# Performance work log

Hardware: AMD Instinct MI355X
Metric: run time of the kernel (lower is better)

The kernel has to match this reference:

```python
import jax, jax.numpy as jnp
import numpy as np

N, D_IN, D_OUT, RANK, MAX_LORAS = 4096, 2048, 2048, 16, 32


def setup_inputs() -> dict:
    key = jax.random.key(0)
    ks = jax.random.split(key, 6)
    x = jax.random.normal(ks[0], (N, D_IN), dtype=jnp.float32)
    adapter_ids = jax.random.randint(ks[1], (N,), 0, MAX_LORAS, dtype=jnp.int32)
    W_base = jax.random.normal(ks[2], (D_OUT, D_IN), dtype=jnp.float32) * (D_IN ** -0.5)
    b_base = jax.random.normal(ks[3], (D_OUT,), dtype=jnp.float32) * 0.01
    lora_A = jax.random.normal(ks[4], (MAX_LORAS, RANK, D_IN), dtype=jnp.float32) * (D_IN ** -0.5)
    lora_B = jax.random.normal(ks[5], (MAX_LORAS, D_OUT, RANK), dtype=jnp.float32) * (RANK ** -0.5)
    lora_scaling = jnp.ones((MAX_LORAS,), dtype=jnp.float32)
    return {"x": x, "adapter_ids": adapter_ids, "W_base": W_base, "b_base": b_base,
            "lora_A": lora_A, "lora_B": lora_B, "lora_scaling": lora_scaling}


def reference(x, adapter_ids, W_base, b_base, lora_A, lora_B, lora_scaling):
    previous_dtype = x.dtype
    # base_layer(x): dense Linear
    result = x @ W_base.T + b_base                      # [N, D_OUT]
    # lora_A(x, adapter_ids): per-token gathered low-rank down-projection (bgmv)
    A_w = lora_A[adapter_ids]                           # [N, RANK, D_IN]
    A_result = jnp.einsum('ni,nri->nr', x, A_w)         # [N, RANK]
    # lora_B(A_result, adapter_ids): per-token gathered up-projection
    B_w = lora_B[adapter_ids]                           # [N, D_OUT, RANK]
    B_result = jnp.einsum('nr,nor->no', A_result, B_w)  # [N, D_OUT]
    # scaled residual add, per-adapter scaling
    scaling = lora_scaling[adapter_ids][:, None]        # [N, 1]
    result = result + B_result * scaling
    # cast back to input dtype (skip_dtype_convert=False)
    return result.astype(previous_dtype)
```

## Files before the change

kernel.cpp:

```cpp
#include <hip/hip_runtime.h>
#include <hip/hip_bf16.h>
#include <stdint.h>

#define NTOK 4096
#define DIN  2048
#define DOUT 2048
#define RANK 16
#define NLORA 32
#define LCAP 512

typedef __attribute__((ext_vector_type(4))) float f32x4;
typedef __attribute__((ext_vector_type(8))) _Float16 f16x8;

typedef const __attribute__((address_space(1))) void* gas_ptr;
typedef __attribute__((address_space(3))) void* las_ptr;

__global__ __launch_bounds__(256)
void prep_kernel(const float* __restrict__ x, const int* __restrict__ ids,
                 const float* __restrict__ W, const float* __restrict__ lA,
                 const float* __restrict__ lB,
                 _Float16* __restrict__ xh, _Float16* __restrict__ wh,
                 _Float16* __restrict__ lAh, _Float16* __restrict__ lBh,
                 int* __restrict__ list, int* __restrict__ counts) {
    const int bid = blockIdx.x;
    if (bid < 7168) {
        const float* src; _Float16* dst; int lb;
        if      (bid < 2048) { src = W;  dst = wh;  lb = bid; }
        else if (bid < 6144) { src = x;  dst = xh;  lb = bid - 2048; }
        else if (bid < 6656) { src = lA; dst = lAh; lb = bid - 6144; }
        else                 { src = lB; dst = lBh; lb = bid - 6656; }
        const size_t i = ((size_t)lb * 256 + threadIdx.x) * 8;
        f32x4 a = *(const f32x4*)(src + i);
        f32x4 b = *(const f32x4*)(src + i + 4);
        f16x8 h;
        h[0] = (_Float16)a.x; h[1] = (_Float16)a.y; h[2] = (_Float16)a.z; h[3] = (_Float16)a.w;
        h[4] = (_Float16)b.x; h[5] = (_Float16)b.y; h[6] = (_Float16)b.z; h[7] = (_Float16)b.w;
        *(f16x8*)(dst + i) = h;
        return;
    }
    const int a = bid - 7168;
    const int wv = threadIdx.x >> 6;
    const int lane = threadIdx.x & 63;
    __shared__ int wcnt[4];
    int c = 0;
    for (int t0 = wv * 1024; t0 < wv * 1024 + 1024; t0 += 64)
        c += __popcll(__ballot(ids[t0 + lane] == a));
    if (lane == 0) wcnt[wv] = c;
    __syncthreads();
    int off = 0;
    for (int w = 0; w < wv; w++) off += wcnt[w];
    if (threadIdx.x == 0) counts[a] = wcnt[0] + wcnt[1] + wcnt[2] + wcnt[3];
    for (int t0 = wv * 1024; t0 < wv * 1024 + 1024; t0 += 64) {
        const int t = t0 + lane;
        const bool m = (ids[t] == a);
        unsigned long long bal = __ballot(m);
        if (m) {
            int pos = off + __popcll(bal & ((1ULL << lane) - 1));
            if (pos < LCAP) list[a * LCAP + pos] = t;
        }
        off += __popcll(bal);
    }
}

__global__ __launch_bounds__(512)
void lora_fused_kernel(const _Float16* __restrict__ xh, const _Float16* __restrict__ lAh,
                       const _Float16* __restrict__ lBh, const float* __restrict__ bias,
                       const float* __restrict__ scal, const int* __restrict__ list,
                       const int* __restrict__ counts, _Float16* __restrict__ Bresh) {
    const int a = blockIdx.x, tile = blockIdx.y;
    const int cnt = counts[a];
    if (tile * 16 >= cnt) return;
    const int wave = threadIdx.x >> 6;
    const int lane = threadIdx.x & 63;
    const int fr = lane & 15, fq = lane >> 4;

    __shared__ float red[8][256];
    __shared__ _Float16 ares_h[16 * 16];

    const int idxA = tile * 16 + fr;
    const int tA = (idxA < cnt) ? list[a * LCAP + idxA] : list[a * LCAP];

    const _Float16* xr = xh + (size_t)tA * DIN + wave * 256 + fq * 8;
    const _Float16* ar = lAh + (size_t)a * RANK * DIN + fr * DIN + wave * 256 + fq * 8;
    f32x4 acc = (f32x4){0.f, 0.f, 0.f, 0.f};
#pragma unroll
    for (int st = 0; st < 8; st++) {
        f16x8 af = *(const f16x8*)(xr + st * 32);
        f16x8 bf = *(const f16x8*)(ar + st * 32);
        acc = __builtin_amdgcn_mfma_f32_16x16x32_f16(af, bf, acc, 0, 0, 0);
    }
#pragma unroll
    for (int j = 0; j < 4; j++) red[wave][lane * 4 + j] = acc[j];
    __syncthreads();
    if (wave == 0) {
        const float s = scal[a];
#pragma unroll
        for (int j = 0; j < 4; j++) {
            float v = 0.f;
#pragma unroll
            for (int w = 0; w < 8; w++) v += red[w][lane * 4 + j];
            ares_h[(fq * 4 + j) * RANK + fr] = (_Float16)(v * s);
        }
    }
    __syncthreads();

    f16x8 af = {};
    if (fq < 2) af = *(const f16x8*)(ares_h + fr * RANK + fq * 8);
    int tj[4];
#pragma unroll
    for (int j = 0; j < 4; j++) {
        const int idx = tile * 16 + fq * 4 + j;
        tj[j] = (idx < cnt) ? list[a * LCAP + idx] : -1;
    }
    const _Float16* Bb = lBh + (size_t)a * DOUT * RANK;
#pragma unroll 4
    for (int oi = 0; oi < 16; oi++) {
        const int o = (wave * 16 + oi) * 16 + fr;
        f16x8 bf = {};
        if (fq < 2) bf = *(const f16x8*)(Bb + (size_t)o * RANK + fq * 8);
        f32x4 c = (f32x4){0.f, 0.f, 0.f, 0.f};
        c = __builtin_amdgcn_mfma_f32_16x16x32_f16(af, bf, c, 0, 0, 0);
        const float bv = bias[o];
#pragma unroll
        for (int j = 0; j < 4; j++)
            if (tj[j] >= 0) Bresh[(size_t)tj[j] * DOUT + o] = (_Float16)(c[j] + bv);
    }
}

#define GBK 64
#define NT (DIN / GBK)

__global__ __launch_bounds__(256, 2)
void gemm_kernel(const _Float16* __restrict__ Ah, const _Float16* __restrict__ Wh,
                 const _Float16* __restrict__ Bresh, float* __restrict__ out) {
    extern __shared__ _Float16 sm[];
    _Float16* As = sm;
    _Float16* Bs = sm + 16384;

    const int tid = threadIdx.x;
    const int wave = tid >> 6;
    const int lane = tid & 63;
    const int wr = wave >> 1, wc = wave & 1;

    const int p = blockIdx.x;
    const int L = (p & 7) * 64 + (p >> 3);
    const int bm = (L >> 4) * 128;
    const int bn = (L & 15) * 128;

    const int rsub = lane >> 3;
    const int cch = (lane & 7) ^ rsub;
    const _Float16* srcA[4];
    const _Float16* srcB[4];
#pragma unroll
    for (int i = 0; i < 4; i++) {
        const int row = (wave * 4 + i) * 8 + rsub;
        srcA[i] = Ah + (size_t)(bm + row) * DIN + cch * 8;
        srcB[i] = Wh + (size_t)(bn + row) * DIN + cch * 8;
    }

    const int fr = lane & 15;
    const int fq = lane >> 4;

    f32x4 acc[4][4];
#pragma unroll
    for (int i = 0; i < 4; i++)
#pragma unroll
        for (int j = 0; j < 4; j++) acc[i][j] = (f32x4){0.f, 0.f, 0.f, 0.f};

#define STAGE(buf, koff)                                                                  \
    do {                                                                                  \
        _Pragma("unroll")                                                                 \
        for (int i = 0; i < 4; i++) {                                                     \
            __builtin_amdgcn_global_load_lds((gas_ptr)(srcA[i] + (koff)),                 \
                (las_ptr)(As + (buf) * 8192 + (wave * 4 + i) * 512), 16, 0, 0);           \
            __builtin_amdgcn_global_load_lds((gas_ptr)(srcB[i] + (koff)),                 \
                (las_ptr)(Bs + (buf) * 8192 + (wave * 4 + i) * 512), 16, 0, 0);           \
        }                                                                                 \
    } while (0)

    STAGE(0, 0);

    for (int kt = 0; kt < NT; ++kt) {
        const int cur = kt & 1;
        if (kt < NT - 1) {
            STAGE(cur ^ 1, (kt + 1) * GBK);
            asm volatile("s_waitcnt vmcnt(8)" ::: "memory");
        } else {
            asm volatile("s_waitcnt vmcnt(0)" ::: "memory");
        }
        __builtin_amdgcn_s_barrier();
        __builtin_amdgcn_sched_barrier(0);

        const _Float16* Ab = As + cur * 8192;
        const _Float16* Bb = Bs + cur * 8192;
#pragma unroll
        for (int kk = 0; kk < 2; kk++) {
            f16x8 av[4], bv[4];
#pragma unroll
            for (int mi = 0; mi < 4; mi++) {
                const int row = wr * 64 + mi * 16 + fr;
                const int slot = (kk * 4 + fq) ^ (row & 7);
                av[mi] = *(const f16x8*)(Ab + row * 64 + slot * 8);
            }
#pragma unroll
            for (int ni = 0; ni < 4; ni++) {
                const int row = wc * 64 + ni * 16 + fr;
                const int slot = (kk * 4 + fq) ^ (row & 7);
                bv[ni] = *(const f16x8*)(Bb + row * 64 + slot * 8);
            }
            __builtin_amdgcn_s_setprio(1);
#pragma unroll
            for (int mi = 0; mi < 4; mi++)
#pragma unroll
                for (int ni = 0; ni < 4; ni++)
                    acc[mi][ni] = __builtin_amdgcn_mfma_f32_16x16x32_f16(av[mi], bv[ni], acc[mi][ni], 0, 0, 0);
            __builtin_amdgcn_s_setprio(0);
        }
        __builtin_amdgcn_s_barrier();
    }

#pragma unroll
    for (int mi = 0; mi < 4; mi++) {
#pragma unroll
        for (int j = 0; j < 4; j++) {
            const int n = bm + wr * 64 + mi * 16 + fq * 4 + j;
#pragma unroll
            for (int ni = 0; ni < 4; ni++) {
                const int o = bn + wc * 64 + ni * 16 + fr;
                out[(size_t)n * DOUT + o] = acc[mi][ni][j] + (float)Bresh[(size_t)n * DOUT + o];
            }
        }
    }
}

extern "C" void kernel_launch(void* const* d_in, const int* in_sizes, int n_in,
                              void* d_out, int out_size, void* d_ws, size_t ws_size,
                              hipStream_t stream) {
    const float* x    = (const float*)d_in[0];
    const int*   ids  = (const int*)d_in[1];
    const float* W    = (const float*)d_in[2];
    const float* bias = (const float*)d_in[3];
    const float* lA   = (const float*)d_in[4];
    const float* lB   = (const float*)d_in[5];
    const float* scal = (const float*)d_in[6];
    float* out = (float*)d_out;

    _Float16* xh    = (_Float16*)d_ws;
    _Float16* wh    = xh + (size_t)NTOK * DIN;
    _Float16* lAh   = wh + (size_t)DOUT * DIN;
    _Float16* lBh   = lAh + (size_t)NLORA * RANK * DIN;
    _Float16* Bresh = lBh + (size_t)NLORA * DOUT * RANK;
    int* list   = (int*)(Bresh + (size_t)NTOK * DOUT);
    int* counts = list + (size_t)NLORA * LCAP;

    prep_kernel<<<dim3(7168 + NLORA), 256, 0, stream>>>(
        x, ids, W, lA, lB, xh, wh, lAh, lBh, list, counts);
    lora_fused_kernel<<<dim3(NLORA, 32), 512, 0, stream>>>(
        xh, lAh, lBh, bias, scal, list, counts, Bresh);
    gemm_kernel<<<dim3(512), 256, 64 * 1024, stream>>>(
        xh, wh, Bresh, out);
}
```

Before: 162.7 us.

## Fuse LoRA into prep kernel and triple-buffer a 256x128 GEMM tile

The token-list build, the fp16 conversion of the LoRA weights and the LoRA down/up projection are merged into one prep kernel. Each LoRA block scans the adapter ids itself and reads fp32 lora_A and lora_B directly, which removes one kernel launch and the intermediate list, count and converted-weight buffers. The base GEMM moves to 512-thread blocks with 256x128 tiles and a three-stage LDS ring (144 KB). Global-to-LDS loads are interleaved between MFMA half-steps with extra barriers. This aims to improve load/compute overlap and reuse of the W tile, at the cost of more barriers, lower occupancy and a redundant serial id scan in every LoRA block.

```diff
diff --git a/kernel.cpp b/kernel.cpp
--- a/kernel.cpp
+++ b/kernel.cpp
@@ -7,7 +7,6 @@
 #define DOUT 2048
 #define RANK 16
 #define NLORA 32
-#define LCAP 512
 
 typedef __attribute__((ext_vector_type(4))) float f32x4;
 typedef __attribute__((ext_vector_type(8))) _Float16 f16x8;
@@ -15,111 +14,100 @@
 typedef const __attribute__((address_space(1))) void* gas_ptr;
 typedef __attribute__((address_space(3))) void* las_ptr;
 
+__device__ __forceinline__ f16x8 cvt2(const float* p) {
+    f32x4 a = *(const f32x4*)(p);
+    f32x4 b = *(const f32x4*)(p + 4);
+    f16x8 h;
+    h[0] = (_Float16)a.x; h[1] = (_Float16)a.y; h[2] = (_Float16)a.z; h[3] = (_Float16)a.w;
+    h[4] = (_Float16)b.x; h[5] = (_Float16)b.y; h[6] = (_Float16)b.z; h[7] = (_Float16)b.w;
+    return h;
+}
+
 __global__ __launch_bounds__(256)
-void prep_kernel(const float* __restrict__ x, const int* __restrict__ ids,
-                 const float* __restrict__ W, const float* __restrict__ lA,
-                 const float* __restrict__ lB,
-                 _Float16* __restrict__ xh, _Float16* __restrict__ wh,
-                 _Float16* __restrict__ lAh, _Float16* __restrict__ lBh,
-                 int* __restrict__ list, int* __restrict__ counts) {
+void prep_lora_kernel(const float* __restrict__ x, const int* __restrict__ ids,
+                      const float* __restrict__ W, const float* __restrict__ lA,
+                      const float* __restrict__ lB, const float* __restrict__ bias,
+                      const float* __restrict__ scal,
+                      _Float16* __restrict__ xh, _Float16* __restrict__ wh,
+                      _Float16* __restrict__ Bresh) {
     const int bid = blockIdx.x;
-    if (bid < 7168) {
+    if (bid >= 1024) {
+        const int b2 = bid - 1024;
         const float* src; _Float16* dst; int lb;
-        if      (bid < 2048) { src = W;  dst = wh;  lb = bid; }
-        else if (bid < 6144) { src = x;  dst = xh;  lb = bid - 2048; }
-        else if (bid < 6656) { src = lA; dst = lAh; lb = bid - 6144; }
-        else                 { src = lB; dst = lBh; lb = bid - 6656; }
+        if (b2 < 2048) { src = W; dst = wh; lb = b2; }
+        else           { src = x; dst = xh; lb = b2 - 2048; }
         const size_t i = ((size_t)lb * 256 + threadIdx.x) * 8;
-        f32x4 a = *(const f32x4*)(src + i);
-        f32x4 b = *(const f32x4*)(src + i + 4);
-        f16x8 h;
-        h[0] = (_Float16)a.x; h[1] = (_Float16)a.y; h[2] = (_Float16)a.z; h[3] = (_Float16)a.w;
-        h[4] = (_Float16)b.x; h[5] = (_Float16)b.y; h[6] = (_Float16)b.z; h[7] = (_Float16)b.w;
-        *(f16x8*)(dst + i) = h;
+        *(f16x8*)(dst + i) = cvt2(src + i);
         return;
     }
-    const int a = bid - 7168;
-    const int wv = threadIdx.x >> 6;
-    const int lane = threadIdx.x & 63;
-    __shared__ int wcnt[4];
-    int c = 0;
-    for (int t0 = wv * 1024; t0 < wv * 1024 + 1024; t0 += 64)
-        c += __popcll(__ballot(ids[t0 + lane] == a));
-    if (lane == 0) wcnt[wv] = c;
+    const int a = bid >> 5, tile = bid & 31;
+    const int wv = threadIdx.x >> 6, lane = threadIdx.x & 63;
+    const int fr = lane & 15, fq = lane >> 4;
+
+    __shared__ int toks[16];
+    __shared__ int scnt;
+    __shared__ float red[4][256];
+    __shared__ _Float16 ares_h[16 * RANK];
+
+    if (wv == 0) {
+        if (lane < 16) toks[lane] = 0;
+        int off = 0;
+        const int lo = tile * 16;
+        for (int t0 = 0; t0 < NTOK; t0 += 64) {
+            const bool m = (ids[t0 + lane] == a);
+            unsigned long long bal = __ballot(m);
+            if (m) {
+                const int pos = off + __popcll(bal & ((1ULL << lane) - 1));
+                if (pos >= lo && pos < lo + 16) toks[pos - lo] = t0 + lane;
+            }
+            off += __popcll(bal);
+        }
+        if (lane == 0) scnt = off;
+    }
     __syncthreads();
-    int off = 0;
-    for (int w = 0; w < wv; w++) off += wcnt[w];
-    if (threadIdx.x == 0) counts[a] = wcnt[0] + wcnt[1] + wcnt[2] + wcnt[3];
-    for (int t0 = wv * 1024; t0 < wv * 1024 + 1024; t0 += 64) {
-        const int t = t0 + lane;
-        const bool m = (ids[t] == a);
-        unsigned long long bal = __ballot(m);
-        if (m) {
-            int pos = off + __popcll(bal & ((1ULL << lane) - 1));
-            if (pos < LCAP) list[a * LCAP + pos] = t;
-        }
-        off += __popcll(bal);
-    }
-}
-
-__global__ __launch_bounds__(512)
-void lora_fused_kernel(const _Float16* __restrict__ xh, const _Float16* __restrict__ lAh,
-                       const _Float16* __restrict__ lBh, const float* __restrict__ bias,
-                       const float* __restrict__ scal, const int* __restrict__ list,
-                       const int* __restrict__ counts, _Float16* __restrict__ Bresh) {
-    const int a = blockIdx.x, tile = blockIdx.y;
-    const int cnt = counts[a];
+    const int cnt = scnt;
     if (tile * 16 >= cnt) return;
-    const int wave = threadIdx.x >> 6;
-    const int lane = threadIdx.x & 63;
-    const int fr = lane & 15, fq = lane >> 4;
-
-    __shared__ float red[8][256];
-    __shared__ _Float16 ares_h[16 * 16];
-
-    const int idxA = tile * 16 + fr;
-    const int tA = (idxA < cnt) ? list[a * LCAP + idxA] : list[a * LCAP];
-
-    const _Float16* xr = xh + (size_t)tA * DIN + wave * 256 + fq * 8;
-    const _Float16* ar = lAh + (size_t)a * RANK * DIN + fr * DIN + wave * 256 + fq * 8;
+
+    const int tA = toks[fr];
+    const float* xr = x + (size_t)tA * DIN + wv * 512 + fq * 8;
+    const float* ar = lA + (size_t)a * RANK * DIN + (size_t)fr * DIN + wv * 512 + fq * 8;
     f32x4 acc = (f32x4){0.f, 0.f, 0.f, 0.f};
 #pragma unroll
-    for (int st = 0; st < 8; st++) {
-        f16x8 af = *(const f16x8*)(xr + st * 32);
-        f16x8 bf = *(const f16x8*)(ar + st * 32);
+    for (int st = 0; st < 16; st++) {
+        f16x8 af = cvt2(xr + st * 32);
+        f16x8 bf = cvt2(ar + st * 32);
         acc = __builtin_amdgcn_mfma_f32_16x16x32_f16(af, bf, acc, 0, 0, 0);
     }
 #pragma unroll
-    for (int j = 0; j < 4; j++) red[wave][lane * 4 + j] = acc[j];
+    for (int j = 0; j < 4; j++) red[wv][lane * 4 + j] = acc[j];
     __syncthreads();
-    if (wave == 0) {
+    if (wv == 0) {
         const float s = scal[a];
 #pragma unroll
         for (int j = 0; j < 4; j++) {
-            float v = 0.f;
-#pragma unroll
-            for (int w = 0; w < 8; w++) v += red[w][lane * 4 + j];
+            float v = red[0][lane * 4 + j] + red[1][lane * 4 + j] +
+                      red[2][lane * 4 + j] + red[3][lane * 4 + j];
             ares_h[(fq * 4 + j) * RANK + fr] = (_Float16)(v * s);
         }
     }
     __syncthreads();
 
-    f16x8 af = {};
-    if (fq < 2) af = *(const f16x8*)(ares_h + fr * RANK + fq * 8);
+    f16x8 af2 = {};
+    if (fq < 2) af2 = *(const f16x8*)(ares_h + fr * RANK + fq * 8);
     int tj[4];
 #pragma unroll
     for (int j = 0; j < 4; j++) {
         const int idx = tile * 16 + fq * 4 + j;
-        tj[j] = (idx < cnt) ? list[a * LCAP + idx] : -1;
-    }
-    const _Float16* Bb = lBh + (size_t)a * DOUT * RANK;
-#pragma unroll 4
-    for (int oi = 0; oi < 16; oi++) {
-        const int o = (wave * 16 + oi) * 16 + fr;
+        tj[j] = (idx < cnt) ? toks[fq * 4 + j] : -1;
+    }
+    const float* Bb = lB + (size_t)a * DOUT * RANK;
+#pragma unroll 2
+    for (int oi = 0; oi < 32; oi++) {
+        const int o = (oi * 4 + wv) * 16 + fr;
         f16x8 bf = {};
-        if (fq < 2) bf = *(const f16x8*)(Bb + (size_t)o * RANK + fq * 8);
+        if (fq < 2) bf = cvt2(Bb + (size_t)o * RANK + fq * 8);
         f32x4 c = (f32x4){0.f, 0.f, 0.f, 0.f};
-        c = __builtin_amdgcn_mfma_f32_16x16x32_f16(af, bf, c, 0, 0, 0);
+        c = __builtin_amdgcn_mfma_f32_16x16x32_f16(af2, bf, c, 0, 0, 0);
         const float bv = bias[o];
 #pragma unroll
         for (int j = 0; j < 4; j++)
@@ -129,13 +117,12 @@
 
 #define GBK 64
 #define NT (DIN / GBK)
-
-__global__ __launch_bounds__(256, 2)
+#define BUFH 24576
+
+__global__ __launch_bounds__(512, 1)
 void gemm_kernel(const _Float16* __restrict__ Ah, const _Float16* __restrict__ Wh,
                  const _Float16* __restrict__ Bresh, float* __restrict__ out) {
     extern __shared__ _Float16 sm[];
-    _Float16* As = sm;
-    _Float16* Bs = sm + 16384;
 
     const int tid = threadIdx.x;
     const int wave = tid >> 6;
@@ -143,18 +130,22 @@
     const int wr = wave >> 1, wc = wave & 1;
 
     const int p = blockIdx.x;
-    const int L = (p & 7) * 64 + (p >> 3);
-    const int bm = (L >> 4) * 128;
+    const int L = (p & 7) * 32 + (p >> 3);
+    const int bm = (L >> 4) * 256;
     const int bn = (L & 15) * 128;
 
     const int rsub = lane >> 3;
     const int cch = (lane & 7) ^ rsub;
     const _Float16* srcA[4];
-    const _Float16* srcB[4];
+    const _Float16* srcB[2];
 #pragma unroll
     for (int i = 0; i < 4; i++) {
         const int row = (wave * 4 + i) * 8 + rsub;
         srcA[i] = Ah + (size_t)(bm + row) * DIN + cch * 8;
+    }
+#pragma unroll
+    for (int i = 0; i < 2; i++) {
+        const int row = (wave * 2 + i) * 8 + rsub;
         srcB[i] = Wh + (size_t)(bn + row) * DIN + cch * 8;
     }
 
@@ -167,56 +158,89 @@
 #pragma unroll
         for (int j = 0; j < 4; j++) acc[i][j] = (f32x4){0.f, 0.f, 0.f, 0.f};
 
-#define STAGE(buf, koff)                                                                  \
-    do {                                                                                  \
-        _Pragma("unroll")                                                                 \
-        for (int i = 0; i < 4; i++) {                                                     \
-            __builtin_amdgcn_global_load_lds((gas_ptr)(srcA[i] + (koff)),                 \
-                (las_ptr)(As + (buf) * 8192 + (wave * 4 + i) * 512), 16, 0, 0);           \
-            __builtin_amdgcn_global_load_lds((gas_ptr)(srcB[i] + (koff)),                 \
-                (las_ptr)(Bs + (buf) * 8192 + (wave * 4 + i) * 512), 16, 0, 0);           \
-        }                                                                                 \
+#define GLDS(srcp, dstp) __builtin_amdgcn_global_load_lds((gas_ptr)(srcp), (las_ptr)(dstp), 16, 0, 0)
+#define STAGE_ALL(buf, koff)                                                           \
+    do {                                                                               \
+        _Pragma("unroll")                                                              \
+        for (int i = 0; i < 4; i++)                                                    \
+            GLDS(srcA[i] + (koff), sm + (buf) * BUFH + (wave * 4 + i) * 512);          \
+        _Pragma("unroll")                                                              \
+        for (int i = 0; i < 2; i++)                                                    \
+            GLDS(srcB[i] + (koff), sm + (buf) * BUFH + 16384 + (wave * 2 + i) * 512);  \
     } while (0)
 
-    STAGE(0, 0);
+    STAGE_ALL(0, 0);
+    STAGE_ALL(1, GBK);
+    asm volatile("s_waitcnt vmcnt(6)" ::: "memory");
+    __builtin_amdgcn_s_barrier();
 
     for (int kt = 0; kt < NT; ++kt) {
-        const int cur = kt & 1;
-        if (kt < NT - 1) {
-            STAGE(cur ^ 1, (kt + 1) * GBK);
-            asm volatile("s_waitcnt vmcnt(8)" ::: "memory");
-        } else {
-            asm volatile("s_waitcnt vmcnt(0)" ::: "memory");
-        }
-        __builtin_amdgcn_s_barrier();
-        __builtin_amdgcn_sched_barrier(0);
-
-        const _Float16* Ab = As + cur * 8192;
-        const _Float16* Bb = Bs + cur * 8192;
+        const _Float16* Ab = sm + (kt % 3) * BUFH;
+        const _Float16* Bb = Ab + 16384;
+        _Float16* Asn = sm + ((kt + 2) % 3) * BUFH;
+        _Float16* Bsn = Asn + 16384;
+        const int kn = (kt + 2) * GBK;
+        const bool doStage = (kt < NT - 2);
+
 #pragma unroll
         for (int kk = 0; kk < 2; kk++) {
             f16x8 av[4], bv[4];
 #pragma unroll
             for (int mi = 0; mi < 4; mi++) {
                 const int row = wr * 64 + mi * 16 + fr;
-                const int slot = (kk * 4 + fq) ^ (row & 7);
-                av[mi] = *(const f16x8*)(Ab + row * 64 + slot * 8);
-            }
-#pragma unroll
-            for (int ni = 0; ni < 4; ni++) {
+                av[mi] = *(const f16x8*)(Ab + row * 64 + (((kk * 4 + fq) ^ (row & 7)) * 8));
+            }
+#pragma unroll
+            for (int ni = 0; ni < 2; ni++) {
                 const int row = wc * 64 + ni * 16 + fr;
-                const int slot = (kk * 4 + fq) ^ (row & 7);
-                bv[ni] = *(const f16x8*)(Bb + row * 64 + slot * 8);
-            }
+                bv[ni] = *(const f16x8*)(Bb + row * 64 + (((kk * 4 + fq) ^ (row & 7)) * 8));
+            }
+            if (doStage) {
+                if (kk == 0) {
+                    GLDS(srcA[0] + kn, Asn + (wave * 4 + 0) * 512);
+                    GLDS(srcA[1] + kn, Asn + (wave * 4 + 1) * 512);
+                } else {
+                    GLDS(srcB[0] + kn, Bsn + (wave * 2 + 0) * 512);
+                    GLDS(srcB[1] + kn, Bsn + (wave * 2 + 1) * 512);
+                }
+            }
+            __builtin_amdgcn_s_barrier();
+            asm volatile("s_waitcnt lgkmcnt(0)" ::: "memory");
+            __builtin_amdgcn_sched_barrier(0);
             __builtin_amdgcn_s_setprio(1);
 #pragma unroll
             for (int mi = 0; mi < 4; mi++)
 #pragma unroll
-                for (int ni = 0; ni < 4; ni++)
+                for (int ni = 0; ni < 2; ni++)
                     acc[mi][ni] = __builtin_amdgcn_mfma_f32_16x16x32_f16(av[mi], bv[ni], acc[mi][ni], 0, 0, 0);
             __builtin_amdgcn_s_setprio(0);
-        }
-        __builtin_amdgcn_s_barrier();
+            __builtin_amdgcn_s_barrier();
+
+#pragma unroll
+            for (int ni = 2; ni < 4; ni++) {
+                const int row = wc * 64 + ni * 16 + fr;
+                bv[ni] = *(const f16x8*)(Bb + row * 64 + (((kk * 4 + fq) ^ (row & 7)) * 8));
+            }
+            if (doStage && kk == 0) {
+                GLDS(srcA[2] + kn, Asn + (wave * 4 + 2) * 512);
+                GLDS(srcA[3] + kn, Asn + (wave * 4 + 3) * 512);
+            }
+            if (kk == 1) {
+                if (kt < NT - 2)       asm volatile("s_waitcnt vmcnt(6)" ::: "memory");
+                else if (kt == NT - 2) asm volatile("s_waitcnt vmcnt(0)" ::: "memory");
+            }
+            __builtin_amdgcn_s_barrier();
+            asm volatile("s_waitcnt lgkmcnt(0)" ::: "memory");
+            __builtin_amdgcn_sched_barrier(0);
+            __builtin_amdgcn_s_setprio(1);
+#pragma unroll
+            for (int mi = 0; mi < 4; mi++)
+#pragma unroll
+                for (int ni = 2; ni < 4; ni++)
+                    acc[mi][ni] = __builtin_amdgcn_mfma_f32_16x16x32_f16(av[mi], bv[ni], acc[mi][ni], 0, 0, 0);
+            __builtin_amdgcn_s_setprio(0);
+            __builtin_amdgcn_s_barrier();
+        }
     }
 
 #pragma unroll
@@ -247,16 +271,10 @@
 
     _Float16* xh    = (_Float16*)d_ws;
     _Float16* wh    = xh + (size_t)NTOK * DIN;
-    _Float16* lAh   = wh + (size_t)DOUT * DIN;
-    _Float16* lBh   = lAh + (size_t)NLORA * RANK * DIN;
-    _Float16* Bresh = lBh + (size_t)NLORA * DOUT * RANK;
-    int* list   = (int*)(Bresh + (size_t)NTOK * DOUT);
-    int* counts = list + (size_t)NLORA * LCAP;
-
-    prep_kernel<<<dim3(7168 + NLORA), 256, 0, stream>>>(
-        x, ids, W, lA, lB, xh, wh, lAh, lBh, list, counts);
-    lora_fused_kernel<<<dim3(NLORA, 32), 512, 0, stream>>>(
-        xh, lAh, lBh, bias, scal, list, counts, Bresh);
-    gemm_kernel<<<dim3(512), 256, 64 * 1024, stream>>>(
+    _Float16* Bresh = wh + (size_t)DOUT * DIN;
+
+    prep_lora_kernel<<<dim3(7168), 256, 0, stream>>>(
+        x, ids, W, lA, lB, bias, scal, xh, wh, Bresh);
+    gemm_kernel<<<dim3(256), 512, 144 * 1024, stream>>>(
         xh, wh, Bresh, out);
 }
```

New measurement: 218.9 us. 34.5% more time.
